# Kernel tuning notes

Measured on AMD Instinct MI355X. Metric: run time of the kernel, lower is better.

Reference implementation:

```python
import jax, jax.numpy as jnp
import numpy as np

N_NODES = 100_000
N_EDGES = 1_000_000
IN_FEAT = 32
ENC = 128          # encoder output = convs[0]/2
C0, C1 = 256, 512  # clf.model.convs
N_CLASSES = 2
EDGE_FEAT = 2


def _linear_params(key, fan_in, fan_out):
    # torch.nn.Linear default init: U(-1/sqrt(fan_in), 1/sqrt(fan_in))
    kw, kb = jax.random.split(key)
    bound = 1.0 / np.sqrt(fan_in)
    w = jax.random.uniform(kw, (fan_in, fan_out), jnp.float32, -bound, bound)
    b = jax.random.uniform(kb, (fan_out,), jnp.float32, -bound, bound)
    return w, b


def setup_inputs() -> dict:
    key = jax.random.key(0)
    ks = jax.random.split(key, 9)
    x = jax.random.normal(ks[0], (N_NODES, IN_FEAT), jnp.float32)
    edge_attr = jax.random.uniform(ks[1], (N_EDGES, EDGE_FEAT), jnp.float32)
    edge_index = jax.random.randint(ks[2], (2, N_EDGES), 0, N_NODES, jnp.int32)
    enc_w, enc_b = _linear_params(ks[3], IN_FEAT, ENC)
    # conv0: in_channels=C0 (feat dim ENC=C0/2)
    e_w0, e_b0 = _linear_params(ks[4], EDGE_FEAT, C0 // 2)
    l_w0, l_b0 = _linear_params(ks[5], C0, C0)
    # conv1: in_channels=C1 (feat dim C0=C1/2)
    e_w1, e_b1 = _linear_params(ks[6], EDGE_FEAT, C1 // 2)
    l_w1, l_b1 = _linear_params(ks[7], C1, C1)
    dec_w, dec_b = _linear_params(ks[8], C1, N_CLASSES)
    return dict(x=x, edge_attr=edge_attr, edge_index=edge_index,
                enc_w=enc_w, enc_b=enc_b,
                e_w0=e_w0, e_b0=e_b0, l_w0=l_w0, l_b0=l_b0,
                e_w1=e_w1, e_b1=e_b1, l_w1=l_w1, l_b1=l_b1,
                dec_w=dec_w, dec_b=dec_b)


def sage_conv(h, edge_attr, src, dst, e_w, e_b, l_w, l_b, n_nodes):
    # edge transform: [E, edge_feat] -> [E, F] where F == h.shape[1]
    ea = edge_attr @ e_w + e_b
    msg = h[src] * ea                                   # gather + multiply, [E, F]
    s = jax.ops.segment_sum(msg, dst, num_segments=n_nodes)
    deg = jax.ops.segment_sum(jnp.ones((src.shape[0], 1), h.dtype), dst,
                              num_segments=n_nodes)
    agg = s / jnp.maximum(deg, 1.0)                     # scatter-mean (0 for isolated)
    return jnp.concatenate([agg, h], axis=1) @ l_w + l_b


def reference(x, edge_attr, edge_index,
              enc_w, enc_b,
              e_w0, e_b0, l_w0, l_b0,
              e_w1, e_b1, l_w1, l_b1,
              dec_w, dec_b):
    src, dst = edge_index[0], edge_index[1]
    n = x.shape[0]
    h = jax.nn.relu(x @ enc_w + enc_b)                  # encoder
    h = sage_conv(h, edge_attr, src, dst, e_w0, e_b0, l_w0, l_b0, n)
    h = jax.nn.relu(h)                                  # relu between conv layers
    h = sage_conv(h, edge_attr, src, dst, e_w1, e_b1, l_w1, l_b1, n)
    h = jax.nn.relu(h)                                  # decoder: relu then linear
    return h @ dec_w + dec_b                            # [N, 2]
```

## Files before the change

### kernel.cpp

```cpp
#include <hip/hip_runtime.h>

#define N_NODES 100000
#define N_EDGES 1000000

typedef __attribute__((ext_vector_type(8))) short bf16x8;
typedef __attribute__((ext_vector_type(4))) float f32x4;

__device__ __forceinline__ void bsplit(float v, unsigned& hi, unsigned& lo) {
  unsigned u = __float_as_uint(v);
  hi = u >> 16;
  float hf = __uint_as_float(hi << 16);
  lo = __float_as_uint(v - hf) >> 16;
}

__global__ __launch_bounds__(256) void zero_kernel(float4* __restrict__ p, long n4) {
  long i = (long)blockIdx.x * 256 + threadIdx.x;
  long stride = (long)gridDim.x * 256;
  float4 z = make_float4(0.f, 0.f, 0.f, 0.f);
  for (; i < n4; i += stride) p[i] = z;
}
__global__ __launch_bounds__(256) void zero_int_kernel(int* __restrict__ p, long n) {
  long i = (long)blockIdx.x * 256 + threadIdx.x;
  long stride = (long)gridDim.x * 256;
  for (; i < n; i += stride) p[i] = 0;
}

__global__ __launch_bounds__(256) void encoder_kernel(
    const float* __restrict__ x, const float* __restrict__ w,
    const float* __restrict__ b, float* __restrict__ h) {
  __shared__ float ws[32 * 128];
  __shared__ float xs[16 * 32];
  __shared__ float bs[128];
  int tid = threadIdx.x;
#pragma unroll
  for (int i = 0; i < 4; ++i)
    reinterpret_cast<float4*>(ws)[tid + i * 256] =
        reinterpret_cast<const float4*>(w)[tid + i * 256];
  if (tid < 128) bs[tid] = b[tid];
  int n0 = blockIdx.x * 16;
  if (tid < 128)
    reinterpret_cast<float4*>(xs)[tid] =
        reinterpret_cast<const float4*>(x + (size_t)n0 * 32)[tid];
  __syncthreads();
  int f = tid & 127;
  int ng = tid >> 7;
#pragma unroll
  for (int i = 0; i < 8; ++i) {
    int nl = ng * 8 + i;
    float acc = bs[f];
#pragma unroll
    for (int k = 0; k < 32; ++k) acc = fmaf(xs[nl * 32 + k], ws[k * 128 + f], acc);
    h[(size_t)(n0 + nl) * 128 + f] = fmaxf(acc, 0.f);
  }
}

__global__ __launch_bounds__(256) void hist_kernel(const int* __restrict__ ei,
                                                   int* __restrict__ deg) {
  int e = blockIdx.x * 256 + threadIdx.x;
  if (e < N_EDGES) atomicAdd(&deg[ei[N_EDGES + e]], 1);
}

__global__ __launch_bounds__(1024) void scan_kernel(const int* __restrict__ deg,
                                                    int* __restrict__ row_start) {
  __shared__ int part[1024];
  int tid = threadIdx.x;
  const int CH = (N_NODES + 1023) / 1024;
  int start = tid * CH;
  int sum = 0;
  for (int i = 0; i < CH; ++i) {
    int idx = start + i;
    if (idx < N_NODES) sum += deg[idx];
  }
  part[tid] = sum;
  __syncthreads();
  for (int off = 1; off < 1024; off <<= 1) {
    int v = (tid >= off) ? part[tid - off] : 0;
    __syncthreads();
    part[tid] += v;
    __syncthreads();
  }
  int prefix = (tid == 0) ? 0 : part[tid - 1];
  for (int i = 0; i < CH; ++i) {
    int idx = start + i;
    if (idx < N_NODES) {
      row_start[idx] = prefix;
      prefix += deg[idx];
    }
  }
}

__global__ __launch_bounds__(256) void fill_kernel(
    const int* __restrict__ ei, const int* __restrict__ row_start,
    int* __restrict__ cursor, int* __restrict__ csr_eidx) {
  int e = blockIdx.x * 256 + threadIdx.x;
  if (e >= N_EDGES) return;
  int d = ei[N_EDGES + e];
  int pos = atomicAdd(&cursor[d], 1);
  csr_eidx[row_start[d] + pos] = e;
}

template <int F>
__global__ __launch_bounds__(256) void aggregate_csr(
    const float* __restrict__ h, const int* __restrict__ row_start,
    const int* __restrict__ deg, const int* __restrict__ csr_eidx,
    const int* __restrict__ ei, const float2* __restrict__ ea2,
    const float* __restrict__ ew, const float* __restrict__ eb,
    float* __restrict__ agg) {
  constexpr int CH = 32;
  __shared__ int ssrc[CH];
  __shared__ float2 sattr[CH];
  __shared__ float sred[F == 128 ? 128 : 1];
  int n = blockIdx.x;
  int tid = threadIdx.x;
  int f = (F == 256) ? tid : (tid & 127);
  int par = (F == 256) ? 0 : (tid >> 7);
  float w0 = ew[f], w1 = ew[F + f], bb = eb[f];
  int rs = row_start[n];
  int dg = deg[n];
  float acc = 0.f;
  for (int j0 = 0; j0 < dg; j0 += CH) {
    int cnt = min(CH, dg - j0);
    __syncthreads();
    if (tid < cnt) {
      int eidx = csr_eidx[rs + j0 + tid];
      ssrc[tid] = ei[eidx];
      sattr[tid] = ea2[eidx];
    }
    __syncthreads();
    if (F == 256) {
      for (int j = 0; j < cnt; ++j) {
        float2 a = sattr[j];
        float eaw = fmaf(a.x, w0, fmaf(a.y, w1, bb));
        acc = fmaf(h[(size_t)ssrc[j] * F + f], eaw, acc);
      }
    } else {
      for (int j = par; j < cnt; j += 2) {
        float2 a = sattr[j];
        float eaw = fmaf(a.x, w0, fmaf(a.y, w1, bb));
        acc = fmaf(h[(size_t)ssrc[j] * F + f], eaw, acc);
      }
    }
  }
  float dinv = 1.f / fmaxf((float)dg, 1.f);
  if (F == 256) {
    agg[(size_t)n * F + f] = acc * dinv;
  } else {
    __syncthreads();
    if (par == 1) sred[f] = acc;
    __syncthreads();
    if (par == 0) agg[(size_t)n * F + f] = (acc + sred[f]) * dinv;
  }
}

template <bool FUSE_DEC>
__global__ __launch_bounds__(512) void gemm2_mfma(
    const float* __restrict__ A1, const float* __restrict__ A2,
    const float* __restrict__ W, const float* __restrict__ bias,
    float* __restrict__ C,
    const float* __restrict__ dw, const float* __restrict__ db,
    float* __restrict__ out, int M, int F, int N) {
  constexpr int BM = 128, BN = 256, BK = 32, LDK = BK + 8;
  __shared__ alignas(16) unsigned short Ah[BM * LDK];
  __shared__ alignas(16) unsigned short Al[BM * LDK];
  __shared__ alignas(16) unsigned short Bh[BN * LDK];
  __shared__ alignas(16) unsigned short Bl[BN * LDK];
  int tid = threadIdx.x;
  int wid = tid >> 6, lane = tid & 63;
  int wm = wid >> 1, wn = wid & 1;
  int lg = lane >> 4, lr = lane & 15;
  int row0 = blockIdx.y * BM;
  int col0 = blockIdx.x * BN;
  f32x4 acc[2][8] = {};

  for (int pass = 0; pass < 2; ++pass) {
    const float* A = pass ? A2 : A1;
    const float* Wp = W + (size_t)pass * F * N;
    for (int k0 = 0; k0 < F; k0 += BK) {
      __syncthreads();
#pragma unroll
      for (int i = 0; i < 2; ++i) {
        int id = tid + i * 512;
        int r = id >> 3, kq = id & 7;
        float4 v = make_float4(0.f, 0.f, 0.f, 0.f);
        int gr = row0 + r;
        if (gr < M) v = *reinterpret_cast<const float4*>(&A[(size_t)gr * F + k0 + kq * 4]);
        unsigned h0, l0, h1, l1, h2, l2, h3, l3;
        bsplit(v.x, h0, l0); bsplit(v.y, h1, l1);
        bsplit(v.z, h2, l2); bsplit(v.w, h3, l3);
        unsigned long long hp = (unsigned long long)h0 | ((unsigned long long)h1 << 16) |
                                ((unsigned long long)h2 << 32) | ((unsigned long long)h3 << 48);
        unsigned long long lp = (unsigned long long)l0 | ((unsigned long long)l1 << 16) |
                                ((unsigned long long)l2 << 32) | ((unsigned long long)l3 << 48);
        *reinterpret_cast<unsigned long long*>(&Ah[r * LDK + kq * 4]) = hp;
        *reinterpret_cast<unsigned long long*>(&Al[r * LDK + kq * 4]) = lp;
      }
#pragma unroll
      for (int i = 0; i < 4; ++i) {
        int id = tid + i * 512;
        int c = id & 255, kq = id >> 8;
        unsigned h0, l0, h1, l1, h2, l2, h3, l3;
        float w0 = Wp[(size_t)(k0 + kq * 4 + 0) * N + col0 + c];
        float w1 = Wp[(size_t)(k0 + kq * 4 + 1) * N + col0 + c];
        float w2 = Wp[(size_t)(k0 + kq * 4 + 2) * N + col0 + c];
        float w3 = Wp[(size_t)(k0 + kq * 4 + 3) * N + col0 + c];
        bsplit(w0, h0, l0); bsplit(w1, h1, l1);
        bsplit(w2, h2, l2); bsplit(w3, h3, l3);
        unsigned long long hp = (unsigned long long)h0 | ((unsigned long long)h1 << 16) |
                                ((unsigned long long)h2 << 32) | ((unsigned long long)h3 << 48);
        unsigned long long lp = (unsigned long long)l0 | ((unsigned long long)l1 << 16) |
                                ((unsigned long long)l2 << 32) | ((unsigned long long)l3 << 48);
        *reinterpret_cast<unsigned long long*>(&Bh[c * LDK + kq * 4]) = hp;
        *reinterpret_cast<unsigned long long*>(&Bl[c * LDK + kq * 4]) = lp;
      }
      __syncthreads();
      bf16x8 ah[2], al[2];
#pragma unroll
      for (int m = 0; m < 2; ++m) {
        int rr = wm * 32 + m * 16 + lr;
        ah[m] = *reinterpret_cast<const bf16x8*>(&Ah[rr * LDK + lg * 8]);
        al[m] = *reinterpret_cast<const bf16x8*>(&Al[rr * LDK + lg * 8]);
      }
#pragma unroll
      for (int n = 0; n < 8; ++n) {
        int cc = wn * 128 + n * 16 + lr;
        bf16x8 bh = *reinterpret_cast<const bf16x8*>(&Bh[cc * LDK + lg * 8]);
        bf16x8 bl = *reinterpret_cast<const bf16x8*>(&Bl[cc * LDK + lg * 8]);
#pragma unroll
        for (int m = 0; m < 2; ++m) {
          acc[m][n] = __builtin_amdgcn_mfma_f32_16x16x32_bf16(ah[m], bh, acc[m][n], 0, 0, 0);
          acc[m][n] = __builtin_amdgcn_mfma_f32_16x16x32_bf16(ah[m], bl, acc[m][n], 0, 0, 0);
          acc[m][n] = __builtin_amdgcn_mfma_f32_16x16x32_bf16(al[m], bh, acc[m][n], 0, 0, 0);
        }
      }
    }
  }
  if (!FUSE_DEC) {
#pragma unroll
    for (int m = 0; m < 2; ++m) {
#pragma unroll
      for (int r = 0; r < 4; ++r) {
        int grow = row0 + wm * 32 + m * 16 + lg * 4 + r;
        if (grow >= M) continue;
#pragma unroll
        for (int n = 0; n < 8; ++n) {
          int gcol = col0 + wn * 128 + n * 16 + lr;
          C[(size_t)grow * N + gcol] = fmaxf(acc[m][n][r] + bias[gcol], 0.f);
        }
      }
    }
  } else {
#pragma unroll
    for (int m = 0; m < 2; ++m) {
#pragma unroll
      for (int r = 0; r < 4; ++r) {
        int grow = row0 + wm * 32 + m * 16 + lg * 4 + r;
        float p0 = 0.f, p1 = 0.f;
#pragma unroll
        for (int n = 0; n < 8; ++n) {
          int gcol = col0 + wn * 128 + n * 16 + lr;
          float v = fmaxf(acc[m][n][r] + bias[gcol], 0.f);
          p0 = fmaf(v, dw[gcol * 2 + 0], p0);
          p1 = fmaf(v, dw[gcol * 2 + 1], p1);
        }
#pragma unroll
        for (int s = 1; s < 16; s <<= 1) {
          p0 += __shfl_xor(p0, s);
          p1 += __shfl_xor(p1, s);
        }
        if (lr == 0 && grow < M) {
          if (wn == 0 && blockIdx.x == 0) { p0 += db[0]; p1 += db[1]; }
          atomicAdd(&out[(size_t)grow * 2 + 0], p0);
          atomicAdd(&out[(size_t)grow * 2 + 1], p1);
        }
      }
    }
  }
}

extern "C" void kernel_launch(void* const* d_in, const int* in_sizes, int n_in,
                              void* d_out, int out_size, void* d_ws, size_t ws_size,
                              hipStream_t stream) {
  const float* x        = (const float*)d_in[0];
  const float* edge_attr= (const float*)d_in[1];
  const int*   ei       = (const int*)d_in[2];
  const float* enc_w    = (const float*)d_in[3];
  const float* enc_b    = (const float*)d_in[4];
  const float* e_w0     = (const float*)d_in[5];
  const float* e_b0     = (const float*)d_in[6];
  const float* l_w0     = (const float*)d_in[7];
  const float* l_b0     = (const float*)d_in[8];
  const float* e_w1     = (const float*)d_in[9];
  const float* e_b1     = (const float*)d_in[10];
  const float* l_w1     = (const float*)d_in[11];
  const float* l_b1     = (const float*)d_in[12];
  const float* dec_w    = (const float*)d_in[13];
  const float* dec_b    = (const float*)d_in[14];
  float* out = (float*)d_out;

  float* ws   = (float*)d_ws;
  float* h0   = ws;
  float* agg0 = h0 + (size_t)N_NODES * 128;
  float* h1   = agg0 + (size_t)N_NODES * 128;
  float* agg1 = ws;
  int* cursor = (int*)agg0;
  int* ip      = (int*)(h1 + (size_t)N_NODES * 256);
  int* deg_i   = ip;
  int* row_s   = ip + N_NODES;
  int* csr_eidx= ip + 2 * N_NODES;
  const float2* ea2 = (const float2*)edge_attr;

  const int M = N_NODES;
  const int ZB = 1024;

  zero_int_kernel<<<ZB, 256, 0, stream>>>(deg_i, N_NODES);
  zero_int_kernel<<<ZB, 256, 0, stream>>>(cursor, N_NODES);

  encoder_kernel<<<N_NODES / 16, 256, 0, stream>>>(x, enc_w, enc_b, h0);
  hist_kernel<<<(N_EDGES + 255) / 256, 256, 0, stream>>>(ei, deg_i);
  scan_kernel<<<1, 1024, 0, stream>>>(deg_i, row_s);
  fill_kernel<<<(N_EDGES + 255) / 256, 256, 0, stream>>>(ei, row_s, cursor, csr_eidx);

  aggregate_csr<128><<<N_NODES, 256, 0, stream>>>(h0, row_s, deg_i, csr_eidx, ei, ea2,
                                                  e_w0, e_b0, agg0);
  gemm2_mfma<false><<<dim3(1, (M + 127) / 128), 512, 0, stream>>>(
      agg0, h0, l_w0, l_b0, h1, nullptr, nullptr, nullptr, M, 128, 256);

  aggregate_csr<256><<<N_NODES, 256, 0, stream>>>(h1, row_s, deg_i, csr_eidx, ei, ea2,
                                                  e_w1, e_b1, agg1);

  zero_kernel<<<ZB, 256, 0, stream>>>((float4*)out, (long)out_size / 4);
  gemm2_mfma<true><<<dim3(2, (M + 127) / 128), 512, 0, stream>>>(
      agg1, h1, l_w1, l_b1, nullptr, dec_w, dec_b, out, M, 256, 512);
}
```

Before: 1.159 ms.

## Store activations as pre-split bf16 hi/lo planes and use wave-per-node aggregation

Producers (encoder, aggregation, layer-0 GEMM epilogue) now write activations as separate bf16 high and low planes. A new transpose kernel pre-splits the weights once per call, so the GEMM loads bf16x8 vectors straight into shared memory instead of converting fp32 in the inner loop. Aggregation switches from one block per node to one wave per node with vectorized gathers and software-prefetched edge indices. The GEMM wave tiling changes to 2x4 with 64x64 per wave. Hi and lo planes together hold the same bytes as fp32, so gather traffic is unchanged, and the gathers become two smaller loads instead of one.

```diff
diff --git a/kernel.cpp b/kernel.cpp
--- a/kernel.cpp
+++ b/kernel.cpp
@@ -5,6 +5,7 @@
 
 typedef __attribute__((ext_vector_type(8))) short bf16x8;
 typedef __attribute__((ext_vector_type(4))) float f32x4;
+typedef unsigned short ushort_t;
 
 __device__ __forceinline__ void bsplit(float v, unsigned& hi, unsigned& lo) {
   unsigned u = __float_as_uint(v);
@@ -27,7 +28,8 @@
 
 __global__ __launch_bounds__(256) void encoder_kernel(
     const float* __restrict__ x, const float* __restrict__ w,
-    const float* __restrict__ b, float* __restrict__ h) {
+    const float* __restrict__ b, ushort_t* __restrict__ hhi,
+    ushort_t* __restrict__ hlo) {
   __shared__ float ws[32 * 128];
   __shared__ float xs[16 * 32];
   __shared__ float bs[128];
@@ -50,7 +52,12 @@
     float acc = bs[f];
 #pragma unroll
     for (int k = 0; k < 32; ++k) acc = fmaf(xs[nl * 32 + k], ws[k * 128 + f], acc);
-    h[(size_t)(n0 + nl) * 128 + f] = fmaxf(acc, 0.f);
+    float v = fmaxf(acc, 0.f);
+    unsigned h_, l_;
+    bsplit(v, h_, l_);
+    size_t idx = (size_t)(n0 + nl) * 128 + f;
+    hhi[idx] = (ushort_t)h_;
+    hlo[idx] = (ushort_t)l_;
   }
 }
 
@@ -99,168 +106,202 @@
   csr_eidx[row_start[d] + pos] = e;
 }
 
+__global__ __launch_bounds__(256) void wsplit_kernel(
+    const float* __restrict__ W, ushort_t* __restrict__ hi,
+    ushort_t* __restrict__ lo, int K2, int N) {
+  __shared__ float t[32][33];
+  int bx = blockIdx.x * 32;
+  int by = blockIdx.y * 32;
+  int lx = threadIdx.x & 31, ly = threadIdx.x >> 5;
+#pragma unroll
+  for (int i = 0; i < 4; ++i)
+    t[ly + i * 8][lx] = W[(size_t)(by + ly + i * 8) * N + bx + lx];
+  __syncthreads();
+#pragma unroll
+  for (int i = 0; i < 4; ++i) {
+    int n_l = ly + i * 8;
+    float v = t[lx][n_l];
+    unsigned h_, l_;
+    bsplit(v, h_, l_);
+    hi[(size_t)(bx + n_l) * K2 + by + lx] = (ushort_t)h_;
+    lo[(size_t)(bx + n_l) * K2 + by + lx] = (ushort_t)l_;
+  }
+}
+
 template <int F>
-__global__ __launch_bounds__(256) void aggregate_csr(
-    const float* __restrict__ h, const int* __restrict__ row_start,
-    const int* __restrict__ deg, const int* __restrict__ csr_eidx,
-    const int* __restrict__ ei, const float2* __restrict__ ea2,
-    const float* __restrict__ ew, const float* __restrict__ eb,
-    float* __restrict__ agg) {
-  constexpr int CH = 32;
-  __shared__ int ssrc[CH];
-  __shared__ float2 sattr[CH];
-  __shared__ float sred[F == 128 ? 128 : 1];
-  int n = blockIdx.x;
-  int tid = threadIdx.x;
-  int f = (F == 256) ? tid : (tid & 127);
-  int par = (F == 256) ? 0 : (tid >> 7);
-  float w0 = ew[f], w1 = ew[F + f], bb = eb[f];
-  int rs = row_start[n];
-  int dg = deg[n];
-  float acc = 0.f;
-  for (int j0 = 0; j0 < dg; j0 += CH) {
-    int cnt = min(CH, dg - j0);
-    __syncthreads();
-    if (tid < cnt) {
-      int eidx = csr_eidx[rs + j0 + tid];
-      ssrc[tid] = ei[eidx];
-      sattr[tid] = ea2[eidx];
-    }
-    __syncthreads();
-    if (F == 256) {
-      for (int j = 0; j < cnt; ++j) {
-        float2 a = sattr[j];
-        float eaw = fmaf(a.x, w0, fmaf(a.y, w1, bb));
-        acc = fmaf(h[(size_t)ssrc[j] * F + f], eaw, acc);
-      }
-    } else {
-      for (int j = par; j < cnt; j += 2) {
-        float2 a = sattr[j];
-        float eaw = fmaf(a.x, w0, fmaf(a.y, w1, bb));
-        acc = fmaf(h[(size_t)ssrc[j] * F + f], eaw, acc);
-      }
-    }
-  }
+__global__ __launch_bounds__(256) void aggregate_ws(
+    const ushort_t* __restrict__ hhi, const ushort_t* __restrict__ hlo,
+    const int* __restrict__ row_start, const int* __restrict__ deg,
+    const int* __restrict__ csr_eidx, const int* __restrict__ ei,
+    const float2* __restrict__ ea2, const float* __restrict__ ew,
+    const float* __restrict__ eb, ushort_t* __restrict__ ahi,
+    ushort_t* __restrict__ alo) {
+  int wid = threadIdx.x >> 6, lane = threadIdx.x & 63;
+  int n = blockIdx.x * 4 + wid;
+  if (n >= N_NODES) return;
+  int rs = row_start[n], dg = deg[n];
   float dinv = 1.f / fmaxf((float)dg, 1.f);
   if (F == 256) {
-    agg[(size_t)n * F + f] = acc * dinv;
+    int f0 = lane * 4;
+    float4 w0 = *reinterpret_cast<const float4*>(&ew[f0]);
+    float4 w1 = *reinterpret_cast<const float4*>(&ew[F + f0]);
+    float4 bb = *reinterpret_cast<const float4*>(&eb[f0]);
+    float a0 = 0.f, a1 = 0.f, a2 = 0.f, a3 = 0.f;
+    int s = 0; float2 at = make_float2(0.f, 0.f);
+    if (dg > 0) { int e = csr_eidx[rs]; s = ei[e]; at = ea2[e]; }
+    for (int j = 0; j < dg; ++j) {
+      int s2 = 0; float2 at2 = make_float2(0.f, 0.f);
+      if (j + 1 < dg) { int e2 = csr_eidx[rs + j + 1]; s2 = ei[e2]; at2 = ea2[e2]; }
+      uint2 uh = *reinterpret_cast<const uint2*>(&hhi[(size_t)s * F + f0]);
+      uint2 ul = *reinterpret_cast<const uint2*>(&hlo[(size_t)s * F + f0]);
+      float v0 = __uint_as_float(uh.x << 16) + __uint_as_float(ul.x << 16);
+      float v1 = __uint_as_float(uh.x & 0xffff0000u) + __uint_as_float(ul.x & 0xffff0000u);
+      float v2 = __uint_as_float(uh.y << 16) + __uint_as_float(ul.y << 16);
+      float v3 = __uint_as_float(uh.y & 0xffff0000u) + __uint_as_float(ul.y & 0xffff0000u);
+      a0 = fmaf(v0, fmaf(at.x, w0.x, fmaf(at.y, w1.x, bb.x)), a0);
+      a1 = fmaf(v1, fmaf(at.x, w0.y, fmaf(at.y, w1.y, bb.y)), a1);
+      a2 = fmaf(v2, fmaf(at.x, w0.z, fmaf(at.y, w1.z, bb.z)), a2);
+      a3 = fmaf(v3, fmaf(at.x, w0.w, fmaf(at.y, w1.w, bb.w)), a3);
+      s = s2; at = at2;
+    }
+    unsigned h_, l_;
+    uint2 oh, ol;
+    bsplit(a0 * dinv, h_, l_); oh.x = h_;        ol.x = l_;
+    bsplit(a1 * dinv, h_, l_); oh.x |= h_ << 16; ol.x |= l_ << 16;
+    bsplit(a2 * dinv, h_, l_); oh.y = h_;        ol.y = l_;
+    bsplit(a3 * dinv, h_, l_); oh.y |= h_ << 16; ol.y |= l_ << 16;
+    *reinterpret_cast<uint2*>(&ahi[(size_t)n * F + f0]) = oh;
+    *reinterpret_cast<uint2*>(&alo[(size_t)n * F + f0]) = ol;
   } else {
-    __syncthreads();
-    if (par == 1) sred[f] = acc;
-    __syncthreads();
-    if (par == 0) agg[(size_t)n * F + f] = (acc + sred[f]) * dinv;
+    int f0 = lane * 2;
+    float2 w0 = *reinterpret_cast<const float2*>(&ew[f0]);
+    float2 w1 = *reinterpret_cast<const float2*>(&ew[F + f0]);
+    float2 bb = *reinterpret_cast<const float2*>(&eb[f0]);
+    float a0 = 0.f, a1 = 0.f;
+    int s = 0; float2 at = make_float2(0.f, 0.f);
+    if (dg > 0) { int e = csr_eidx[rs]; s = ei[e]; at = ea2[e]; }
+    for (int j = 0; j < dg; ++j) {
+      int s2 = 0; float2 at2 = make_float2(0.f, 0.f);
+      if (j + 1 < dg) { int e2 = csr_eidx[rs + j + 1]; s2 = ei[e2]; at2 = ea2[e2]; }
+      unsigned uh = *reinterpret_cast<const unsigned*>(&hhi[(size_t)s * F + f0]);
+      unsigned ul = *reinterpret_cast<const unsigned*>(&hlo[(size_t)s * F + f0]);
+      float v0 = __uint_as_float(uh << 16) + __uint_as_float(ul << 16);
+      float v1 = __uint_as_float(uh & 0xffff0000u) + __uint_as_float(ul & 0xffff0000u);
+      a0 = fmaf(v0, fmaf(at.x, w0.x, fmaf(at.y, w1.x, bb.x)), a0);
+      a1 = fmaf(v1, fmaf(at.x, w0.y, fmaf(at.y, w1.y, bb.y)), a1);
+      s = s2; at = at2;
+    }
+    unsigned h0_, l0_, h1_, l1_;
+    bsplit(a0 * dinv, h0_, l0_);
+    bsplit(a1 * dinv, h1_, l1_);
+    *reinterpret_cast<unsigned*>(&ahi[(size_t)n * F + f0]) = h0_ | (h1_ << 16);
+    *reinterpret_cast<unsigned*>(&alo[(size_t)n * F + f0]) = l0_ | (l1_ << 16);
   }
 }
 
 template <bool FUSE_DEC>
 __global__ __launch_bounds__(512) void gemm2_mfma(
-    const float* __restrict__ A1, const float* __restrict__ A2,
-    const float* __restrict__ W, const float* __restrict__ bias,
-    float* __restrict__ C,
-    const float* __restrict__ dw, const float* __restrict__ db,
-    float* __restrict__ out, int M, int F, int N) {
-  constexpr int BM = 128, BN = 256, BK = 32, LDK = BK + 8;
-  __shared__ alignas(16) unsigned short Ah[BM * LDK];
-  __shared__ alignas(16) unsigned short Al[BM * LDK];
-  __shared__ alignas(16) unsigned short Bh[BN * LDK];
-  __shared__ alignas(16) unsigned short Bl[BN * LDK];
+    const ushort_t* __restrict__ a1hi, const ushort_t* __restrict__ a1lo,
+    const ushort_t* __restrict__ a2hi, const ushort_t* __restrict__ a2lo,
+    const ushort_t* __restrict__ wthi, const ushort_t* __restrict__ wtlo,
+    const float* __restrict__ bias, ushort_t* __restrict__ chi,
+    ushort_t* __restrict__ clo, const float* __restrict__ dw,
+    const float* __restrict__ db, float* __restrict__ out, int M, int F, int N) {
+  constexpr int LDK = 40;
+  __shared__ alignas(16) ushort_t Ah[128 * LDK];
+  __shared__ alignas(16) ushort_t Al[128 * LDK];
+  __shared__ alignas(16) ushort_t Bh[256 * LDK];
+  __shared__ alignas(16) ushort_t Bl[256 * LDK];
   int tid = threadIdx.x;
   int wid = tid >> 6, lane = tid & 63;
-  int wm = wid >> 1, wn = wid & 1;
+  int wm = wid >> 2, wn = wid & 3;
   int lg = lane >> 4, lr = lane & 15;
-  int row0 = blockIdx.y * BM;
-  int col0 = blockIdx.x * BN;
-  f32x4 acc[2][8] = {};
+  int row0 = blockIdx.y * 128;
+  int col0 = blockIdx.x * 256;
+  int K2 = 2 * F;
+  f32x4 acc[4][4] = {};
+  int ar = tid >> 2, ag = tid & 3;
 
   for (int pass = 0; pass < 2; ++pass) {
-    const float* A = pass ? A2 : A1;
-    const float* Wp = W + (size_t)pass * F * N;
-    for (int k0 = 0; k0 < F; k0 += BK) {
+    const ushort_t* Ahg = pass ? a2hi : a1hi;
+    const ushort_t* Alg = pass ? a2lo : a1lo;
+    for (int k0 = 0; k0 < F; k0 += 32) {
       __syncthreads();
+      {
+        int gr = row0 + ar;
+        bf16x8 vh = {}, vl = {};
+        if (gr < M) {
+          vh = *reinterpret_cast<const bf16x8*>(&Ahg[(size_t)gr * F + k0 + ag * 8]);
+          vl = *reinterpret_cast<const bf16x8*>(&Alg[(size_t)gr * F + k0 + ag * 8]);
+        }
+        *reinterpret_cast<bf16x8*>(&Ah[ar * LDK + ag * 8]) = vh;
+        *reinterpret_cast<bf16x8*>(&Al[ar * LDK + ag * 8]) = vl;
+      }
+      int kk = pass * F + k0;
 #pragma unroll
       for (int i = 0; i < 2; ++i) {
         int id = tid + i * 512;
-        int r = id >> 3, kq = id & 7;
-        float4 v = make_float4(0.f, 0.f, 0.f, 0.f);
-        int gr = row0 + r;
-        if (gr < M) v = *reinterpret_cast<const float4*>(&A[(size_t)gr * F + k0 + kq * 4]);
-        unsigned h0, l0, h1, l1, h2, l2, h3, l3;
-        bsplit(v.x, h0, l0); bsplit(v.y, h1, l1);
-        bsplit(v.z, h2, l2); bsplit(v.w, h3, l3);
-        unsigned long long hp = (unsigned long long)h0 | ((unsigned long long)h1 << 16) |
-                                ((unsigned long long)h2 << 32) | ((unsigned long long)h3 << 48);
-        unsigned long long lp = (unsigned long long)l0 | ((unsigned long long)l1 << 16) |
-                                ((unsigned long long)l2 << 32) | ((unsigned long long)l3 << 48);
-        *reinterpret_cast<unsigned long long*>(&Ah[r * LDK + kq * 4]) = hp;
-        *reinterpret_cast<unsigned long long*>(&Al[r * LDK + kq * 4]) = lp;
-      }
-#pragma unroll
-      for (int i = 0; i < 4; ++i) {
-        int id = tid + i * 512;
-        int c = id & 255, kq = id >> 8;
-        unsigned h0, l0, h1, l1, h2, l2, h3, l3;
-        float w0 = Wp[(size_t)(k0 + kq * 4 + 0) * N + col0 + c];
-        float w1 = Wp[(size_t)(k0 + kq * 4 + 1) * N + col0 + c];
-        float w2 = Wp[(size_t)(k0 + kq * 4 + 2) * N + col0 + c];
-        float w3 = Wp[(size_t)(k0 + kq * 4 + 3) * N + col0 + c];
-        bsplit(w0, h0, l0); bsplit(w1, h1, l1);
-        bsplit(w2, h2, l2); bsplit(w3, h3, l3);
-        unsigned long long hp = (unsigned long long)h0 | ((unsigned long long)h1 << 16) |
-                                ((unsigned long long)h2 << 32) | ((unsigned long long)h3 << 48);
-        unsigned long long lp = (unsigned long long)l0 | ((unsigned long long)l1 << 16) |
-                                ((unsigned long long)l2 << 32) | ((unsigned long long)l3 << 48);
-        *reinterpret_cast<unsigned long long*>(&Bh[c * LDK + kq * 4]) = hp;
-        *reinterpret_cast<unsigned long long*>(&Bl[c * LDK + kq * 4]) = lp;
+        int c = id >> 2, g = id & 3;
+        *reinterpret_cast<bf16x8*>(&Bh[c * LDK + g * 8]) =
+            *reinterpret_cast<const bf16x8*>(&wthi[(size_t)(col0 + c) * K2 + kk + g * 8]);
+        *reinterpret_cast<bf16x8*>(&Bl[c * LDK + g * 8]) =
+            *reinterpret_cast<const bf16x8*>(&wtlo[(size_t)(col0 + c) * K2 + kk + g * 8]);
       }
       __syncthreads();
-      bf16x8 ah[2], al[2];
-#pragma unroll
-      for (int m = 0; m < 2; ++m) {
-        int rr = wm * 32 + m * 16 + lr;
-        ah[m] = *reinterpret_cast<const bf16x8*>(&Ah[rr * LDK + lg * 8]);
-        al[m] = *reinterpret_cast<const bf16x8*>(&Al[rr * LDK + lg * 8]);
-      }
-#pragma unroll
-      for (int n = 0; n < 8; ++n) {
-        int cc = wn * 128 + n * 16 + lr;
-        bf16x8 bh = *reinterpret_cast<const bf16x8*>(&Bh[cc * LDK + lg * 8]);
-        bf16x8 bl = *reinterpret_cast<const bf16x8*>(&Bl[cc * LDK + lg * 8]);
-#pragma unroll
-        for (int m = 0; m < 2; ++m) {
-          acc[m][n] = __builtin_amdgcn_mfma_f32_16x16x32_bf16(ah[m], bh, acc[m][n], 0, 0, 0);
-          acc[m][n] = __builtin_amdgcn_mfma_f32_16x16x32_bf16(ah[m], bl, acc[m][n], 0, 0, 0);
-          acc[m][n] = __builtin_amdgcn_mfma_f32_16x16x32_bf16(al[m], bh, acc[m][n], 0, 0, 0);
+      bf16x8 fah[4], fal[4];
+#pragma unroll
+      for (int m = 0; m < 4; ++m) {
+        int rr = wm * 64 + m * 16 + lr;
+        fah[m] = *reinterpret_cast<const bf16x8*>(&Ah[rr * LDK + lg * 8]);
+        fal[m] = *reinterpret_cast<const bf16x8*>(&Al[rr * LDK + lg * 8]);
+      }
+#pragma unroll
+      for (int nn = 0; nn < 4; ++nn) {
+        int cc = wn * 64 + nn * 16 + lr;
+        bf16x8 fbh = *reinterpret_cast<const bf16x8*>(&Bh[cc * LDK + lg * 8]);
+        bf16x8 fbl = *reinterpret_cast<const bf16x8*>(&Bl[cc * LDK + lg * 8]);
+#pragma unroll
+        for (int m = 0; m < 4; ++m) {
+          acc[m][nn] = __builtin_amdgcn_mfma_f32_16x16x32_bf16(fah[m], fbh, acc[m][nn], 0, 0, 0);
+          acc[m][nn] = __builtin_amdgcn_mfma_f32_16x16x32_bf16(fah[m], fbl, acc[m][nn], 0, 0, 0);
+          acc[m][nn] = __builtin_amdgcn_mfma_f32_16x16x32_bf16(fal[m], fbh, acc[m][nn], 0, 0, 0);
         }
       }
     }
   }
   if (!FUSE_DEC) {
 #pragma unroll
-    for (int m = 0; m < 2; ++m) {
+    for (int m = 0; m < 4; ++m) {
 #pragma unroll
       for (int r = 0; r < 4; ++r) {
-        int grow = row0 + wm * 32 + m * 16 + lg * 4 + r;
+        int grow = row0 + wm * 64 + m * 16 + lg * 4 + r;
         if (grow >= M) continue;
 #pragma unroll
-        for (int n = 0; n < 8; ++n) {
-          int gcol = col0 + wn * 128 + n * 16 + lr;
-          C[(size_t)grow * N + gcol] = fmaxf(acc[m][n][r] + bias[gcol], 0.f);
+        for (int nn = 0; nn < 4; ++nn) {
+          int gcol = col0 + wn * 64 + nn * 16 + lr;
+          float v = fmaxf(acc[m][nn][r] + bias[gcol], 0.f);
+          unsigned h_, l_;
+          bsplit(v, h_, l_);
+          chi[(size_t)grow * N + gcol] = (ushort_t)h_;
+          clo[(size_t)grow * N + gcol] = (ushort_t)l_;
         }
       }
     }
   } else {
 #pragma unroll
-    for (int m = 0; m < 2; ++m) {
+    for (int m = 0; m < 4; ++m) {
 #pragma unroll
       for (int r = 0; r < 4; ++r) {
-        int grow = row0 + wm * 32 + m * 16 + lg * 4 + r;
+        int grow = row0 + wm * 64 + m * 16 + lg * 4 + r;
         float p0 = 0.f, p1 = 0.f;
-#pragma unroll
-        for (int n = 0; n < 8; ++n) {
-          int gcol = col0 + wn * 128 + n * 16 + lr;
-          float v = fmaxf(acc[m][n][r] + bias[gcol], 0.f);
-          p0 = fmaf(v, dw[gcol * 2 + 0], p0);
-          p1 = fmaf(v, dw[gcol * 2 + 1], p1);
+        if (grow < M) {
+#pragma unroll
+          for (int nn = 0; nn < 4; ++nn) {
+            int gcol = col0 + wn * 64 + nn * 16 + lr;
+            float v = fmaxf(acc[m][nn][r] + bias[gcol], 0.f);
+            p0 = fmaf(v, dw[gcol * 2 + 0], p0);
+            p1 = fmaf(v, dw[gcol * 2 + 1], p1);
+          }
         }
 #pragma unroll
         for (int s = 1; s < 16; s <<= 1) {
@@ -297,16 +338,23 @@
   const float* dec_b    = (const float*)d_in[14];
   float* out = (float*)d_out;
 
-  float* ws   = (float*)d_ws;
-  float* h0   = ws;
-  float* agg0 = h0 + (size_t)N_NODES * 128;
-  float* h1   = agg0 + (size_t)N_NODES * 128;
-  float* agg1 = ws;
-  int* cursor = (int*)agg0;
-  int* ip      = (int*)(h1 + (size_t)N_NODES * 256);
-  int* deg_i   = ip;
-  int* row_s   = ip + N_NODES;
-  int* csr_eidx= ip + 2 * N_NODES;
+  char* base = (char*)d_ws;
+  ushort_t* h0hi   = (ushort_t*)(base);
+  ushort_t* h0lo   = (ushort_t*)(base + 25600000);
+  ushort_t* agg0hi = (ushort_t*)(base + 51200000);
+  ushort_t* agg0lo = (ushort_t*)(base + 76800000);
+  ushort_t* h1hi   = (ushort_t*)(base + 102400000);
+  ushort_t* h1lo   = (ushort_t*)(base + 153600000);
+  ushort_t* wt0hi  = (ushort_t*)(base + 204800000);
+  ushort_t* wt0lo  = wt0hi + 256 * 256;
+  ushort_t* wt1hi  = wt0lo + 256 * 256;
+  ushort_t* wt1lo  = wt1hi + 512 * 512;
+  int* deg_i    = (int*)(base + 206200000);
+  int* row_s    = deg_i + N_NODES;
+  int* csr_eidx = row_s + N_NODES;
+  int* cursor   = (int*)agg0hi;
+  ushort_t* agg1hi = (ushort_t*)(base);
+  ushort_t* agg1lo = (ushort_t*)(base + 51200000);
   const float2* ea2 = (const float2*)edge_attr;
 
   const int M = N_NODES;
@@ -315,20 +363,25 @@
   zero_int_kernel<<<ZB, 256, 0, stream>>>(deg_i, N_NODES);
   zero_int_kernel<<<ZB, 256, 0, stream>>>(cursor, N_NODES);
 
-  encoder_kernel<<<N_NODES / 16, 256, 0, stream>>>(x, enc_w, enc_b, h0);
+  encoder_kernel<<<N_NODES / 16, 256, 0, stream>>>(x, enc_w, enc_b, h0hi, h0lo);
   hist_kernel<<<(N_EDGES + 255) / 256, 256, 0, stream>>>(ei, deg_i);
   scan_kernel<<<1, 1024, 0, stream>>>(deg_i, row_s);
   fill_kernel<<<(N_EDGES + 255) / 256, 256, 0, stream>>>(ei, row_s, cursor, csr_eidx);
 
-  aggregate_csr<128><<<N_NODES, 256, 0, stream>>>(h0, row_s, deg_i, csr_eidx, ei, ea2,
-                                                  e_w0, e_b0, agg0);
+  wsplit_kernel<<<dim3(8, 8), 256, 0, stream>>>(l_w0, wt0hi, wt0lo, 256, 256);
+  wsplit_kernel<<<dim3(16, 16), 256, 0, stream>>>(l_w1, wt1hi, wt1lo, 512, 512);
+
+  aggregate_ws<128><<<N_NODES / 4, 256, 0, stream>>>(h0hi, h0lo, row_s, deg_i, csr_eidx,
+                                                     ei, ea2, e_w0, e_b0, agg0hi, agg0lo);
   gemm2_mfma<false><<<dim3(1, (M + 127) / 128), 512, 0, stream>>>(
-      agg0, h0, l_w0, l_b0, h1, nullptr, nullptr, nullptr, M, 128, 256);
-
-  aggregate_csr<256><<<N_NODES, 256, 0, stream>>>(h1, row_s, deg_i, csr_eidx, ei, ea2,
-                                                  e_w1, e_b1, agg1);
+      agg0hi, agg0lo, h0hi, h0lo, wt0hi, wt0lo, l_b0, h1hi, h1lo,
+      nullptr, nullptr, nullptr, M, 128, 256);
+
+  aggregate_ws<256><<<N_NODES / 4, 256, 0, stream>>>(h1hi, h1lo, row_s, deg_i, csr_eidx,
+                                                     ei, ea2, e_w1, e_b1, agg1hi, agg1lo);
 
   zero_kernel<<<ZB, 256, 0, stream>>>((float4*)out, (long)out_size / 4);
   gemm2_mfma<true><<<dim3(2, (M + 127) / 128), 512, 0, stream>>>(
-      agg1, h1, l_w1, l_b1, nullptr, dec_w, dec_b, out, M, 256, 512);
-}
+      agg1hi, agg1lo, h1hi, h1lo, wt1hi, wt1lo, l_b1, nullptr, nullptr,
+      dec_w, dec_b, out, M, 256, 512);
+}
```

Measured after the change: 1.197 ms. 3.2% more time.
